# Kernel tuning notes

Measured on AMD Instinct MI355X. Metric: run time of the kernel, lower is better.

The kernel has to match this reference:

```python
import jax, jax.numpy as jnp
import numpy as np

N = 1536       # n_nodes
D_IN = 256     # in_features
D_OUT = 64     # out_features (= n_hidden, n_heads=1, is_concat=True)
N_WAY = 16     # known_attacks_count
SLOPE = 0.2    # LeakyReLU negative slope


def setup_inputs() -> dict:
    key = jax.random.key(0)
    k1, k2, k3, k4, k5 = jax.random.split(key, 5)
    hidden_vectors = jax.random.normal(k1, (N, D_IN), dtype=jnp.float32)
    labels = jax.random.randint(k2, (N, 1), 0, N_WAY)
    zda_mask = jax.random.randint(k3, (N, 1), 0, 2).astype(bool)
    # deterministic support/query split: first half support, last half query
    query_mask = jnp.concatenate([jnp.zeros(N // 2, bool), jnp.ones(N // 2, bool)])
    W = jax.random.normal(k4, (D_OUT, D_IN), jnp.float32) * (1.0 / np.sqrt(D_IN))
    attn_w = jax.random.normal(k5, (D_OUT,), jnp.float32) * (1.0 / np.sqrt(D_OUT))
    return {"hidden_vectors": hidden_vectors, "W": W, "attn_w": attn_w,
            "labels": labels, "zda_mask": zda_mask, "query_mask": query_mask,
            "known_attacks_count": N_WAY}


def _forward(hidden_vectors, W, attn_w, labels, zda_mask, n_way):
    n = hidden_vectors.shape[0]
    dt = hidden_vectors.dtype
    # one-hot labels (scatter equivalent)
    oh = jax.nn.one_hot(labels[:, 0], n_way, dtype=dt)                 # [n, n_way]
    known = ~zda_mask[:, 0]                                            # unknown == zda
    ohm = jnp.where(known[:, None], oh, jnp.zeros((), dt))             # masked one-hot
    # collaborative kernel: semantic similarity between known pairs, else 1
    sem = ohm @ ohm.T                                                  # [n, n]
    cond = known[:, None] & known[None, :]
    kernel = jnp.where(cond, sem, jnp.ones((), dt))
    # GATv2 with shared weights, 1 head: e[i,j] = attn . lrelu(g[i] + g[j])
    g = hidden_vectors @ W.T                                           # [n, d_out]
    s = g[:, None, :] + g[None, :, :]                                  # [n, n, d_out]
    s = jnp.where(s >= 0, s, SLOPE * s)                                # LeakyReLU
    e = jnp.einsum('ijd,d->ij', s, attn_w)                             # [n, n]
    e = jnp.where(kernel == 0.0, -jnp.inf, e)                          # colaborative mask
    a = jax.nn.softmax(e, axis=1)                                      # [n, n]
    h_out = a @ g                                                      # [n, d_out] (concat, 1 head)
    # centroids over support nodes (first half)
    n_sup = n // 2
    h_sup, oh_sup = h_out[:n_sup], oh[:n_sup]
    agg = oh_sup.T @ h_sup                                             # [n_way, d_out]
    counts = oh_sup.sum(0)                                             # [n_way]
    centroids = jnp.where((counts > 0)[:, None],
                          agg / jnp.maximum(counts, 1.0)[:, None], 0.0)
    # inverse euclidean distance scores for query nodes (last half)
    hq = h_out[n_sup:]
    d2 = (jnp.sum(hq * hq, 1)[:, None] + jnp.sum(centroids * centroids, 1)[None, :]
          - 2.0 * hq @ centroids.T)
    dist = jnp.sqrt(jnp.maximum(d2, 0.0))
    scores = 1.0 / (dist + 1e-10)
    return scores, h_out, a


def reference(hidden_vectors, W, attn_w, labels, zda_mask, query_mask, known_attacks_count):
    return _forward(hidden_vectors, W, attn_w, labels, zda_mask, known_attacks_count)
```

## Files before the change

### kernel.cpp

```cpp
#include <hip/hip_runtime.h>
#include <math.h>

#define NN 1536
#define DIN 256
#define DOUT 64
#define NWAY 16
#define NSUP 768
#define IB 12

#define OFF_SCORES 0
#define OFF_H 12288
#define OFF_A 110592

#define WG 0
#define WQ 98304
#define WCODE 99840
#define WCENT 101376
#define WHP 102400

__global__ __launch_bounds__(256) void k_g(const float* __restrict__ hid,
                                           const float* __restrict__ W,
                                           const float* __restrict__ attw,
                                           const int* __restrict__ labels,
                                           const int* __restrict__ zda,
                                           float* __restrict__ g,
                                           float* __restrict__ q,
                                           int* __restrict__ code) {
  int t = threadIdx.x;
  int r = t >> 6, d = t & 63;
  int i = blockIdx.x * 4 + r;
  const float4* hp = (const float4*)(hid + (size_t)i * DIN);
  const float4* wp = (const float4*)(W + (size_t)d * DIN);
  float4 acc = {0.f, 0.f, 0.f, 0.f};
#pragma unroll
  for (int k = 0; k < DIN / 4; k++) {
    float4 h4 = hp[k];
    float4 w4 = wp[k];
    acc.x = fmaf(h4.x, w4.x, acc.x);
    acc.y = fmaf(h4.y, w4.y, acc.y);
    acc.z = fmaf(h4.z, w4.z, acc.z);
    acc.w = fmaf(h4.w, w4.w, acc.w);
  }
  float gv = (acc.x + acc.y) + (acc.z + acc.w);
  g[(size_t)i * DOUT + d] = gv;
  float val = gv * attw[d];
#pragma unroll
  for (int off = 32; off >= 1; off >>= 1) val += __shfl_xor(val, off, 64);
  if (d == 0) q[i] = 0.6f * val;
  if (t < 4) {
    int ii = blockIdx.x * 4 + t;
    code[ii] = zda[ii] ? -1 : labels[ii];
  }
}

__global__ __launch_bounds__(256, 2) void k_e(const float* __restrict__ g,
                                              const float* __restrict__ q,
                                              const int* __restrict__ code,
                                              const float* __restrict__ attw,
                                              float* __restrict__ aout) {
  __shared__ float gi[IB * DOUT];
  __shared__ float qi[IB];
  __shared__ int ci[IB];
  int t = threadIdx.x;
  int i0 = blockIdx.x * IB;
  int j = blockIdx.y * 256 + t;

  if (t < IB * 16) {
    ((float4*)gi)[t] = ((const float4*)(g + (size_t)i0 * DOUT))[t];
  } else if (t < IB * 16 + IB) {
    int u = t - IB * 16;
    qi[u] = q[i0 + u];
    ci[u] = code[i0 + u];
  }
  float4 gj[16];
  const float4* gp = (const float4*)(g + (size_t)j * DOUT);
#pragma unroll
  for (int k = 0; k < 16; k++) gj[k] = gp[k];
  float qj = q[j];
  int cj = code[j];
  __syncthreads();

  const float4* wv = (const float4*)attw;
#pragma unroll 1
  for (int u = 0; u < IB; u++) {
    const float4* gv = (const float4*)(gi + u * DOUT);
    float4 acc = {0.f, 0.f, 0.f, 0.f};
#pragma unroll
    for (int k = 0; k < 16; k++) {
      float4 a4 = gv[k];
      float4 w4 = wv[k];
      float4 b4 = gj[k];
      acc.x = fmaf(w4.x, fabsf(a4.x + b4.x), acc.x);
      acc.y = fmaf(w4.y, fabsf(a4.y + b4.y), acc.y);
      acc.z = fmaf(w4.z, fabsf(a4.z + b4.z), acc.z);
      acc.w = fmaf(w4.w, fabsf(a4.w + b4.w), acc.w);
    }
    float e = (qi[u] + qj) + 0.4f * ((acc.x + acc.y) + (acc.z + acc.w));
    int cu = ci[u];
    if ((cu >= 0) && (cj >= 0) && (cu != cj)) e = -1e30f;
    aout[(size_t)(i0 + u) * NN + j] = e;
  }
}

__global__ __launch_bounds__(256) void k_sm(float* __restrict__ a) {
  __shared__ float red[8];
  int i = blockIdx.x, t = threadIdx.x;
  float* row = a + (size_t)i * NN;
  float v[6];
#pragma unroll
  for (int k = 0; k < 6; k++) v[k] = row[t + 256 * k];
  float m = v[0];
#pragma unroll
  for (int k = 1; k < 6; k++) m = fmaxf(m, v[k]);
#pragma unroll
  for (int off = 32; off >= 1; off >>= 1) m = fmaxf(m, __shfl_xor(m, off, 64));
  int w = t >> 6;
  if ((t & 63) == 0) red[w] = m;
  __syncthreads();
  m = fmaxf(fmaxf(red[0], red[1]), fmaxf(red[2], red[3]));
  float s = 0.f;
#pragma unroll
  for (int k = 0; k < 6; k++) {
    v[k] = __expf(v[k] - m);
    s += v[k];
  }
#pragma unroll
  for (int off = 32; off >= 1; off >>= 1) s += __shfl_xor(s, off, 64);
  if ((t & 63) == 0) red[4 + w] = s;
  __syncthreads();
  s = (red[4] + red[5]) + (red[6] + red[7]);
  float inv = 1.f / s;
#pragma unroll
  for (int k = 0; k < 6; k++) row[t + 256 * k] = v[k] * inv;
}

__global__ __launch_bounds__(256) void k_h(const float* __restrict__ a,
                                           const float* __restrict__ g,
                                           float* __restrict__ hp) {
  __shared__ float at[16 * 132];
  __shared__ float gl[128 * 64];
  int t = threadIdx.x;
  int jc = blockIdx.y;
  int r0 = blockIdx.x * 16;
#pragma unroll
  for (int u = 0; u < 2; u++) {
    int f4 = t + u * 256;
    int row = f4 >> 5;
    int col4 = f4 & 31;
    float4 v = *(const float4*)(a + (size_t)(r0 + row) * NN + jc * 128 + col4 * 4);
    *(float4*)(at + row * 132 + col4 * 4) = v;
  }
  {
    const float4* src = (const float4*)(g + (size_t)jc * 128 * DOUT);
    float4* dst = (float4*)gl;
#pragma unroll
    for (int u = 0; u < 8; u++) dst[t + u * 256] = src[t + u * 256];
  }
  __syncthreads();
  int r = t >> 4;
  int dq = (t & 15) * 4;
  const float4* ap = (const float4*)(at + r * 132);
  float4 acc = {0.f, 0.f, 0.f, 0.f};
  for (int j4 = 0; j4 < 32; j4++) {
    float4 av = ap[j4];
    const float* gb = gl + (j4 * 4) * 64 + dq;
    float4 g0 = *(const float4*)(gb);
    float4 g1 = *(const float4*)(gb + 64);
    float4 g2 = *(const float4*)(gb + 128);
    float4 g3 = *(const float4*)(gb + 192);
    acc.x = fmaf(av.x, g0.x, acc.x); acc.y = fmaf(av.x, g0.y, acc.y);
    acc.z = fmaf(av.x, g0.z, acc.z); acc.w = fmaf(av.x, g0.w, acc.w);
    acc.x = fmaf(av.y, g1.x, acc.x); acc.y = fmaf(av.y, g1.y, acc.y);
    acc.z = fmaf(av.y, g1.z, acc.z); acc.w = fmaf(av.y, g1.w, acc.w);
    acc.x = fmaf(av.z, g2.x, acc.x); acc.y = fmaf(av.z, g2.y, acc.y);
    acc.z = fmaf(av.z, g2.z, acc.z); acc.w = fmaf(av.z, g2.w, acc.w);
    acc.x = fmaf(av.w, g3.x, acc.x); acc.y = fmaf(av.w, g3.y, acc.y);
    acc.z = fmaf(av.w, g3.z, acc.z); acc.w = fmaf(av.w, g3.w, acc.w);
  }
  *(float4*)(hp + ((size_t)jc * NN + r0 + r) * DOUT + dq) = acc;
}

__global__ __launch_bounds__(256) void k_hred(const float* __restrict__ hp,
                                              float* __restrict__ h) {
  int idx = blockIdx.x * 256 + threadIdx.x;
  float s = 0.f;
#pragma unroll
  for (int c = 0; c < 12; c++) s += hp[(size_t)c * (NN * DOUT) + idx];
  h[idx] = s;
}

__global__ __launch_bounds__(1024) void k_cent(const float* __restrict__ h,
                                               const int* __restrict__ labels,
                                               float* __restrict__ cent) {
  __shared__ float part[16][64];
  __shared__ int pc[16];
  int c = blockIdx.x, t = threadIdx.x;
  int d = t & 63, rq = t >> 6;
  float acc = 0.f;
  int cnt = 0;
#pragma unroll 4
  for (int r = rq; r < NSUP; r += 16) {
    int lab = labels[r];
    if (lab == c) { acc += h[(size_t)r * DOUT + d]; cnt++; }
  }
  part[rq][d] = acc;
  if (d == 0) pc[rq] = cnt;
  __syncthreads();
  if (t < 64) {
    float num = 0.f;
    int count = 0;
#pragma unroll
    for (int k = 0; k < 16; k++) { num += part[k][t]; count += pc[k]; }
    cent[c * DOUT + t] = (count > 0) ? (num / (float)count) : 0.f;
  }
}

__global__ __launch_bounds__(256) void k_scores(const float* __restrict__ h,
                                                const float* __restrict__ cent,
                                                float* __restrict__ scores) {
  __shared__ float cl[NWAY * 65];
  __shared__ float hl[16 * 65];
  int t = threadIdx.x;
  int q0 = blockIdx.x * 16;
#pragma unroll
  for (int u = 0; u < 4; u++) {
    int f = t + u * 256;
    int row = f >> 6, k = f & 63;
    cl[row * 65 + k] = cent[f];
    hl[row * 65 + k] = h[(size_t)(NSUP + q0) * DOUT + f];
  }
  __syncthreads();
  int qr = t >> 4, c = t & 15;
  const float* hv = hl + qr * 65;
  const float* cv = cl + c * 65;
  float hh = 0.f, cc = 0.f, hc = 0.f;
#pragma unroll
  for (int k = 0; k < DOUT; k++) {
    float av = hv[k], bv = cv[k];
    hh = fmaf(av, av, hh);
    cc = fmaf(bv, bv, cc);
    hc = fmaf(av, bv, hc);
  }
  float d2 = fmaxf(hh + cc - 2.f * hc, 0.f);
  scores[q0 * NWAY + t] = 1.f / (sqrtf(d2) + 1e-10f);
}

extern "C" void kernel_launch(void* const* d_in, const int* in_sizes, int n_in,
                              void* d_out, int out_size, void* d_ws, size_t ws_size,
                              hipStream_t stream) {
  const float* hid = (const float*)d_in[0];
  const float* W = (const float*)d_in[1];
  const float* attw = (const float*)d_in[2];
  const int* labels = (const int*)d_in[3];
  const int* zda = (const int*)d_in[4];
  float* out = (float*)d_out;
  float* ws = (float*)d_ws;

  float* g = ws + WG;
  float* q = ws + WQ;
  int* code = (int*)(ws + WCODE);
  float* cent = ws + WCENT;
  float* hp = ws + WHP;
  float* scores = out + OFF_SCORES;
  float* h = out + OFF_H;
  float* a = out + OFF_A;

  hipLaunchKernelGGL(k_g, dim3(NN / 4), dim3(256), 0, stream, hid, W, attw, labels, zda, g, q, code);
  hipLaunchKernelGGL(k_e, dim3(NN / IB, NN / 256), dim3(256), 0, stream, g, q, code, attw, a);
  hipLaunchKernelGGL(k_sm, dim3(NN), dim3(256), 0, stream, a);
  hipLaunchKernelGGL(k_h, dim3(NN / 16, NN / 128), dim3(256), 0, stream, a, g, hp);
  hipLaunchKernelGGL(k_hred, dim3(NN * DOUT / 256), dim3(256), 0, stream, hp, h);
  hipLaunchKernelGGL(k_cent, dim3(NWAY), dim3(1024), 0, stream, h, labels, cent);
  hipLaunchKernelGGL(k_scores, dim3(NSUP / 16), dim3(256), 0, stream, h, cent, scores);
}
```

Before: 87.11 us.

## Split k_e feature dimension across wave pairs with LDS partial-sum reduction

The pairwise attention-logit kernel now divides the 64-wide feature dot product between two waves, so each thread holds 8 float4 of g[j] instead of 16. That halves register pressure and raises the launch-bounds occupancy hint from 2 to 3. Partial sums go through a new LDS buffer and a second pass combines them, applies the mask and writes the output. Each block now covers 128 columns, so the grid doubles. This adds an extra barrier, more LDS traffic and more blocks that each reload the i-row data.

```diff
diff --git a/kernel.cpp b/kernel.cpp
--- a/kernel.cpp
+++ b/kernel.cpp
@@ -7,6 +7,7 @@
 #define NWAY 16
 #define NSUP 768
 #define IB 12
+#define JBLK 128
 
 #define OFF_SCORES 0
 #define OFF_H 12288
@@ -53,40 +54,44 @@
   }
 }
 
-__global__ __launch_bounds__(256, 2) void k_e(const float* __restrict__ g,
+__global__ __launch_bounds__(256, 3) void k_e(const float* __restrict__ g,
                                               const float* __restrict__ q,
                                               const int* __restrict__ code,
                                               const float* __restrict__ attw,
                                               float* __restrict__ aout) {
-  __shared__ float gi[IB * DOUT];
+  __shared__ float gis[IB * DOUT];
+  __shared__ float lds_p[4][IB][64];
   __shared__ float qi[IB];
   __shared__ int ci[IB];
   int t = threadIdx.x;
+  int lane = t & 63;
+  int w = t >> 6;
+  int whalf = __builtin_amdgcn_readfirstlane(w & 1);
+  int jhi = w >> 1;
   int i0 = blockIdx.x * IB;
-  int j = blockIdx.y * 256 + t;
+  int j0 = blockIdx.y * JBLK;
+  int j = j0 + jhi * 64 + lane;
 
   if (t < IB * 16) {
-    ((float4*)gi)[t] = ((const float4*)(g + (size_t)i0 * DOUT))[t];
+    ((float4*)gis)[t] = ((const float4*)(g + (size_t)i0 * DOUT))[t];
   } else if (t < IB * 16 + IB) {
     int u = t - IB * 16;
     qi[u] = q[i0 + u];
     ci[u] = code[i0 + u];
   }
-  float4 gj[16];
-  const float4* gp = (const float4*)(g + (size_t)j * DOUT);
-#pragma unroll
-  for (int k = 0; k < 16; k++) gj[k] = gp[k];
-  float qj = q[j];
-  int cj = code[j];
-  __syncthreads();
-
-  const float4* wv = (const float4*)attw;
+  float4 gj[8];
+  const float4* gp = (const float4*)(g + (size_t)j * DOUT + whalf * 32);
+#pragma unroll
+  for (int k = 0; k < 8; k++) gj[k] = gp[k];
+  const float4* wv = (const float4*)(attw + whalf * 32);
+  __syncthreads();
+
 #pragma unroll 1
   for (int u = 0; u < IB; u++) {
-    const float4* gv = (const float4*)(gi + u * DOUT);
+    const float4* gv = (const float4*)(gis + u * DOUT + whalf * 32);
     float4 acc = {0.f, 0.f, 0.f, 0.f};
 #pragma unroll
-    for (int k = 0; k < 16; k++) {
+    for (int k = 0; k < 8; k++) {
       float4 a4 = gv[k];
       float4 w4 = wv[k];
       float4 b4 = gj[k];
@@ -95,10 +100,25 @@
       acc.z = fmaf(w4.z, fabsf(a4.z + b4.z), acc.z);
       acc.w = fmaf(w4.w, fabsf(a4.w + b4.w), acc.w);
     }
-    float e = (qi[u] + qj) + 0.4f * ((acc.x + acc.y) + (acc.z + acc.w));
+    lds_p[w][u][lane] = (acc.x + acc.y) + (acc.z + acc.w);
+  }
+  __syncthreads();
+
+  int jl = t & 127;
+  int sb = (jl >> 6) * 2;
+  int ll = jl & 63;
+  int jg = j0 + jl;
+  float qj = q[jg];
+  int cj = code[jg];
+  int u0 = (t >> 7) * 6;
+#pragma unroll
+  for (int v = 0; v < 6; v++) {
+    int u = u0 + v;
+    float s = lds_p[sb][u][ll] + lds_p[sb + 1][u][ll];
+    float e = (qi[u] + qj) + 0.4f * s;
     int cu = ci[u];
     if ((cu >= 0) && (cj >= 0) && (cu != cj)) e = -1e30f;
-    aout[(size_t)(i0 + u) * NN + j] = e;
+    aout[(size_t)(i0 + u) * NN + jg] = e;
   }
 }
 
@@ -266,7 +286,7 @@
   float* a = out + OFF_A;
 
   hipLaunchKernelGGL(k_g, dim3(NN / 4), dim3(256), 0, stream, hid, W, attw, labels, zda, g, q, code);
-  hipLaunchKernelGGL(k_e, dim3(NN / IB, NN / 256), dim3(256), 0, stream, g, q, code, attw, a);
+  hipLaunchKernelGGL(k_e, dim3(NN / IB, NN / JBLK), dim3(256), 0, stream, g, q, code, attw, a);
   hipLaunchKernelGGL(k_sm, dim3(NN), dim3(256), 0, stream, a);
   hipLaunchKernelGGL(k_h, dim3(NN / 16, NN / 128), dim3(256), 0, stream, a, g, hp);
   hipLaunchKernelGGL(k_hred, dim3(NN * DOUT / 256), dim3(256), 0, stream, hp, h);
```

After: 77.62 us. 10.9% less time.
